# Optimization experiments

Hardware: AMD Instinct MI355X
Metric: run time of the kernel (lower is better)

## Reference

```python
import jax, jax.numpy as jnp
import numpy as np

NUM_HEADS = 16
B, S, H = 2, 8192, 1024


def setup_inputs() -> dict:
    key = jax.random.key(0)
    ks = jax.random.split(key, 6)
    scale = 1.0 / np.sqrt(H)
    return {
        "hidden_states": jax.random.normal(ks[0], (B, S, H), dtype=jnp.float32),
        "Wq": jax.random.normal(ks[1], (H, H), dtype=jnp.float32) * scale,
        "Wk": jax.random.normal(ks[2], (H, H), dtype=jnp.float32) * scale,
        "Wv": jax.random.normal(ks[3], (H, H), dtype=jnp.float32) * scale,
        "Wg": jax.random.normal(ks[4], (H, H), dtype=jnp.float32) * scale,
        "Wo": jax.random.normal(ks[5], (H, H), dtype=jnp.float32) * scale,
        "gamma": jnp.ones((H,), dtype=jnp.float32),
        "beta": jnp.zeros((H,), dtype=jnp.float32),
    }


def reference(hidden_states, Wq, Wk, Wv, Wg, Wo, gamma, beta):
    b, s, h = hidden_states.shape
    nh = NUM_HEADS
    dk = h // nh
    dv = h // nh
    # projections (bias-free linears)
    q = (hidden_states @ Wq).reshape(b, s, nh, dk)
    k = (hidden_states @ Wk).reshape(b, s, nh, dk)
    v = (hidden_states @ Wv).reshape(b, s, nh, dv)
    g = hidden_states @ Wg  # [b, s, h]
    # elu+1 feature map
    q = jax.nn.elu(q) + 1.0
    k = jax.nn.elu(k) + 1.0
    # kv = k outer v per token, then contracted with q  ==> (q.k) * v (no [b,h,n,d,e] tensor)
    qk = jnp.sum(q * k, axis=-1, keepdims=True)        # [b, s, nh, 1]
    k_sum = jnp.sum(k, axis=1, keepdims=True)          # [b, 1, nh, dk] (global over seq)
    normalizer = jnp.sum(q * k_sum, axis=-1, keepdims=True)  # [b, s, nh, 1]
    z = qk * v / (normalizer + 1e-6)                   # [b, s, nh, dv]
    z = z.reshape(b, s, nh * dv)
    # LayerNorm (eps=1e-5, affine)
    mu = jnp.mean(z, axis=-1, keepdims=True)
    var = jnp.mean(jnp.square(z - mu), axis=-1, keepdims=True)
    z = (z - mu) * jax.lax.rsqrt(var + 1e-5) * gamma + beta
    # SiLU gating and output projection
    z = z * jax.nn.silu(g)
    return z @ Wo
```

## Files before the change

kernel.cpp:

```cpp
#include <hip/hip_runtime.h>


typedef unsigned short ushort_t;
typedef unsigned int uint_t;

using short8  = __attribute__((ext_vector_type(8))) short;
using floatx4 = __attribute__((ext_vector_type(4))) float;

#define HDIM  1024
#define T_TOK 16384
#define KSPLIT 3072

__device__ __forceinline__ ushort_t f2bf(float f) {
    uint_t u = __builtin_bit_cast(uint_t, f);
    u = (u + 0x7fff + ((u >> 16) & 1)) >> 16;
    return (ushort_t)u;
}
__device__ __forceinline__ float bf2f(ushort_t h) {
    uint_t u = ((uint_t)h) << 16;
    return __builtin_bit_cast(float, u);
}
__device__ __forceinline__ void split2(float f, ushort_t& hi, ushort_t& lo) {
    hi = f2bf(f);
    lo = f2bf(f - bf2f(hi));
}
__device__ __forceinline__ void gload_lds16(const ushort_t* g, ushort_t* l) {
    __builtin_amdgcn_global_load_lds(
        (const __attribute__((address_space(1))) void*)g,
        (__attribute__((address_space(3))) void*)l, 16, 0, 0);
}

__global__ void split_w(const float* __restrict__ W0, const float* __restrict__ W1,
                        const float* __restrict__ W2, const float* __restrict__ W3,
                        const float* __restrict__ W4, ushort_t* __restrict__ WT2) {
    __shared__ float tile[32][33];
    const int z = blockIdx.z;
    const float* W = (z == 0) ? W0 : (z == 1) ? W1 : (z == 2) ? W2 : (z == 3) ? W3 : W4;
    ushort_t* dst = WT2 + (size_t)z * HDIM * 2048;
    const int n0 = blockIdx.x * 32, k0 = blockIdx.y * 32;
    const int tx = threadIdx.x & 31, ty0 = threadIdx.x >> 5;
#pragma unroll
    for (int s = 0; s < 4; ++s) {
        int ty = ty0 + 8 * s;
        tile[ty][tx] = W[(size_t)(k0 + ty) * HDIM + n0 + tx];
    }
    __syncthreads();
#pragma unroll
    for (int s = 0; s < 4; ++s) {
        int ty = ty0 + 8 * s;
        float v = tile[tx][ty];
        ushort_t hi, lo;
        split2(v, hi, lo);
        dst[(size_t)(n0 + ty) * 2048 + k0 + tx] = hi;
        dst[(size_t)(n0 + ty) * 2048 + 1024 + k0 + tx] = lo;
    }
}

__global__ __launch_bounds__(256)
void split_hidden(const float* __restrict__ h, ushort_t* __restrict__ Hs) {
    const int t = blockIdx.x;
    const int c = threadIdx.x;
    const float4 x = ((const float4*)(h + (size_t)t * HDIM))[c];
    ushort_t hi[4], lo[4];
    split2(x.x, hi[0], lo[0]); split2(x.y, hi[1], lo[1]);
    split2(x.z, hi[2], lo[2]); split2(x.w, hi[3], lo[3]);
    ushort_t* row = Hs + (size_t)t * 2048;
    uint2 hp, lp;
    hp.x = (uint_t)hi[0] | ((uint_t)hi[1] << 16);
    hp.y = (uint_t)hi[2] | ((uint_t)hi[3] << 16);
    lp.x = (uint_t)lo[0] | ((uint_t)lo[1] << 16);
    lp.y = (uint_t)lo[2] | ((uint_t)lo[3] << 16);
    *(uint2*)(row + c * 4) = hp;
    *(uint2*)(row + 1024 + c * 4) = lp;
}


#define FENCE() asm volatile("" ::: "memory")
#define VMW4()  asm volatile("s_waitcnt vmcnt(4)" ::: "memory")

#define STG_A(t, h, bsel) do { \
    const int ka_ = ((t) * 64 >= 2048) ? ((t) * 64 - 2048) : ((t) * 64); \
    gload_lds16(Ag + (size_t)((h) * 128) * 2048 + ka_, \
                &As[(bsel) * 16384 + ((h) * 128 + w * 16) * 64]); \
    gload_lds16(Ag + (size_t)((h) * 128 + 8) * 2048 + ka_, \
                &As[(bsel) * 16384 + ((h) * 128 + w * 16 + 8) * 64]); \
  } while (0)

#define STG_B(t, h, bsel) do { \
    const int kb_ = ((t) * 64 >= 1024) ? ((t) * 64 - 1024) : ((t) * 64); \
    gload_lds16(Bg + (size_t)((h) * 128) * 2048 + kb_, \
                &Bs[(bsel) * 16384 + ((h) * 128 + w * 16) * 64]); \
    gload_lds16(Bg + (size_t)((h) * 128 + 8) * 2048 + kb_, \
                &Bs[(bsel) * 16384 + ((h) * 128 + w * 16 + 8) * 64]); \
  } while (0)

#define RD_A(dst, bsel, mb, kc) do { \
    const ushort_t* _pa = ((kc) ? Ar1 : Ar0) + (bsel) * 16384; \
    _Pragma("unroll") \
    for (int _i = 0; _i < 4; ++_i) \
        dst[_i] = *(const short8*)(_pa + ((mb) + _i) * 1024); \
  } while (0)

#define RD_B(dst, bsel, kc) do { \
    const ushort_t* _pb = ((kc) ? Br1 : Br0) + (bsel) * 16384; \
    _Pragma("unroll") \
    for (int _j = 0; _j < 4; ++_j) \
        dst[_j] = *(const short8*)(_pb + _j * 1024); \
  } while (0)

#define MMX(mb, a, b) do { \
    __builtin_amdgcn_s_setprio(1); \
    _Pragma("unroll") \
    for (int _i = 0; _i < 4; ++_i) \
    _Pragma("unroll") \
    for (int _j = 0; _j < 4; ++_j) \
        acc[(mb) + _i][_j] = __builtin_amdgcn_mfma_f32_16x16x32_bf16( \
            a[_i], b[_j], acc[(mb) + _i][_j], 0, 0, 0); \
    __builtin_amdgcn_s_setprio(0); \
  } while (0)

#define TILE(t, bsel) do { \
     \
    RD_A(afB, bsel, 4, 0); \
    STG_A((t) + 1, 0, (bsel) ^ 1); STG_A((t) + 1, 1, (bsel) ^ 1); \
    MMX(0, afA, bfv0); \
     \
    RD_A(afA, bsel, 0, 1); \
    RD_B(bfv1, bsel, 1); \
    MMX(4, afB, bfv0); \
     \
    RD_A(afB, bsel, 4, 1); \
    MMX(0, afA, bfv1); \
     \
    __builtin_amdgcn_sched_barrier(0); \
    asm volatile("s_waitcnt lgkmcnt(0)" ::: "memory"); \
    FENCE(); __builtin_amdgcn_s_barrier(); FENCE(); \
    STG_B((t) + 2, 0, bsel); STG_B((t) + 2, 1, bsel); \
    VMW4(); \
    FENCE(); __builtin_amdgcn_s_barrier(); FENCE(); \
    __builtin_amdgcn_sched_barrier(0); \
     \
    RD_A(afA, (bsel) ^ 1, 0, 0); \
    RD_B(bfv0, (bsel) ^ 1, 0); \
    MMX(4, afB, bfv1); \
  } while (0)

template <int EPI>
__global__ __launch_bounds__(512, 2)
void gemm256(const ushort_t* __restrict__ A, const ushort_t* __restrict__ Bw,
             float* __restrict__ D, const float* __restrict__ kf,
             const float* __restrict__ ksum, float* __restrict__ scbuf,
             ushort_t* __restrict__ zbuf, const float* __restrict__ gamma,
             const float* __restrict__ beta) {
    __shared__ ushort_t As[2 * 256 * 64];
    __shared__ ushort_t Bs[2 * 256 * 64];
    const int tid = threadIdx.x;
    const int bx = blockIdx.x, by = blockIdx.y;
    const int w = tid >> 6, lane = tid & 63;
    const int wm = w & 1, wn = w >> 1;
    const int lrow = lane & 15, lq = lane >> 4;

    const int srow = lane >> 3;
    const int scol = ((lane & 7) ^ srow) * 8;
    const ushort_t* Ag = A + (size_t)(bx * 256 + w * 16 + srow) * 2048 + scol;
    const ushort_t* Bg = Bw + (size_t)(by * 256 + w * 16 + srow) * 2048 + scol;

    const int c0 = (lq ^ (lrow & 7)) * 8;
    const int c1 = ((lq + 4) ^ (lrow & 7)) * 8;
    const ushort_t* Ar0 = As + (wm * 128 + lrow) * 64 + c0;
    const ushort_t* Ar1 = As + (wm * 128 + lrow) * 64 + c1;
    const ushort_t* Br0 = Bs + (wn * 64 + lrow) * 64 + c0;
    const ushort_t* Br1 = Bs + (wn * 64 + lrow) * 64 + c1;

    floatx4 acc[8][4] = {};
    short8 afA[4], afB[4], bfv0[4], bfv1[4];

    STG_A(0, 0, 0); STG_A(0, 1, 0);
    STG_B(0, 0, 0); STG_B(0, 1, 0);
    STG_B(1, 0, 1); STG_B(1, 1, 1);
    VMW4();
    FENCE(); __builtin_amdgcn_s_barrier(); FENCE();
    __builtin_amdgcn_sched_barrier(0);
    RD_A(afA, 0, 0, 0);
    RD_B(bfv0, 0, 0);

#pragma unroll 1
    for (int t = 0; t < 48; t += 2) {
        TILE(t, 0);
        TILE(t + 1, 1);
    }

    const int rowbase = bx * 256 + wm * 128 + lq * 4;
    const int colbase = by * 256 + wn * 64 + lrow;

    if constexpr (EPI == 0 || EPI == 2) {
#pragma unroll
        for (int i = 0; i < 8; ++i)
#pragma unroll
            for (int j = 0; j < 4; ++j) {
                const int col = colbase + j * 16;
#pragma unroll
                for (int r = 0; r < 4; ++r) {
                    const int row = rowbase + i * 16 + r;
                    float val = acc[i][j][r];
                    if (EPI == 0) val = (val > 0.0f) ? (val + 1.0f) : (expm1f(val) + 1.0f);
                    D[(size_t)row * HDIM + col] = val;
                }
            }
    } else if constexpr (EPI == 1) {
        const int b = bx >> 5;
        float ksv[4];
#pragma unroll
        for (int j = 0; j < 4; ++j) ksv[j] = ksum[b * HDIM + colbase + j * 16];
        const int h = by * 4 + wn;
#pragma unroll
        for (int i = 0; i < 8; ++i)
#pragma unroll
            for (int r = 0; r < 4; ++r) {
                const int row = rowbase + i * 16 + r;
                float qk = 0.f, nm = 0.f;
#pragma unroll
                for (int j = 0; j < 4; ++j) {
                    float qv = acc[i][j][r];
                    qv = (qv > 0.0f) ? (qv + 1.0f) : (expm1f(qv) + 1.0f);
                    const float kv = kf[(size_t)row * HDIM + colbase + j * 16];
                    qk += qv * kv;
                    nm += qv * ksv[j];
                }
#pragma unroll
                for (int off = 1; off < 16; off <<= 1) {
                    qk += __shfl_xor(qk, off, 64);
                    nm += __shfl_xor(nm, off, 64);
                }
                if (lrow == 0) scbuf[row * 16 + h] = qk / (nm + 1e-6f);
            }
    } else {
#pragma unroll
        for (int i = 0; i < 8; ++i)
#pragma unroll
            for (int j = 0; j < 4; ++j) {
                const int col = colbase + j * 16;
                const float gam = gamma[col], bet = beta[col];
#pragma unroll
                for (int r = 0; r < 4; ++r) {
                    const int row = rowbase + i * 16 + r;
                    ushort_t* zr = zbuf + (size_t)row * 2048;
                    const float zn = bf2f(zr[col]) + bf2f(zr[1024 + col]);
                    const float g = acc[i][j][r];
                    const float sg = g / (1.0f + expf(-g));
                    ushort_t hi, lo;
                    split2((zn * gam + bet) * sg, hi, lo);
                    zr[col] = hi;
                    zr[1024 + col] = lo;
                }
            }
    }
}

template <int EPI>
__global__ __launch_bounds__(256)
void gemm_swz(const ushort_t* __restrict__ A, const ushort_t* __restrict__ Bw,
              float* __restrict__ D, const float* __restrict__ kf,
              const float* __restrict__ ksum, float* __restrict__ scbuf,
              ushort_t* __restrict__ zbuf) {
    __shared__ ushort_t As[128 * 64];
    __shared__ ushort_t Bs[128 * 64];
    const int tid = threadIdx.x;
    const int bx = blockIdx.x, by = blockIdx.y;
    const int w = tid >> 6, lane = tid & 63;
    const int wm = w & 1, wn = w >> 1;
    const int lrow = lane & 15, lq = lane >> 4;

    const int srow = lane >> 3;
    const int scol = ((lane & 7) ^ srow) * 8;
    const ushort_t* Ag = A + (size_t)(bx * 128 + w * 32 + srow) * 2048 + scol;
    const ushort_t* Bg = Bw + (size_t)(by * 128 + w * 32 + srow) * 2048 + scol;

    floatx4 acc[4][4] = {};

    for (int k0 = 0; k0 < KSPLIT; k0 += 64) {
        const int ka = k0 - ((k0 >= 2048) ? 2048 : 0);
        const int kb = k0 - ((k0 >= 1024) ? 1024 : 0);
        __syncthreads();
#pragma unroll
        for (int n = 0; n < 4; ++n) {
            gload_lds16(Ag + (size_t)(n * 8) * 2048 + ka, &As[(w * 32 + n * 8) * 64]);
            gload_lds16(Bg + (size_t)(n * 8) * 2048 + kb, &Bs[(w * 32 + n * 8) * 64]);
        }
        __syncthreads();
#pragma unroll
        for (int kk = 0; kk < 64; kk += 32) {
            short8 af[4], bf[4];
#pragma unroll
            for (int i = 0; i < 4; ++i) {
                const int c = (((kk >> 3) + lq) ^ (lrow & 7)) * 8;
                af[i] = *(const short8*)&As[(wm * 64 + i * 16 + lrow) * 64 + c];
            }
#pragma unroll
            for (int j = 0; j < 4; ++j) {
                const int c = (((kk >> 3) + lq) ^ (lrow & 7)) * 8;
                bf[j] = *(const short8*)&Bs[(wn * 64 + j * 16 + lrow) * 64 + c];
            }
#pragma unroll
            for (int i = 0; i < 4; ++i)
#pragma unroll
                for (int j = 0; j < 4; ++j)
                    acc[i][j] = __builtin_amdgcn_mfma_f32_16x16x32_bf16(af[i], bf[j], acc[i][j], 0, 0, 0);
        }
    }

    const int rowbase = bx * 128 + wm * 64 + lq * 4;
    const int colbase = by * 128 + wn * 64 + lrow;
#pragma unroll
    for (int i = 0; i < 4; ++i)
#pragma unroll
        for (int j = 0; j < 4; ++j) {
            const int col = colbase + j * 16;
#pragma unroll
            for (int r = 0; r < 4; ++r) {
                const int row = rowbase + i * 16 + r;
                float val = acc[i][j][r];
                if (EPI == 0) val = (val > 0.0f) ? (val + 1.0f) : (expm1f(val) + 1.0f);
                D[(size_t)row * HDIM + col] = val;
            }
        }
}

__global__ void ksum_partial(const float* __restrict__ kf, float* __restrict__ partial) {
    const int rg = blockIdx.x;
    const int tid = threadIdx.x;
    const float4* p = (const float4*)(kf + (size_t)rg * 64 * HDIM) + tid;
    float4 s = {0.f, 0.f, 0.f, 0.f};
    for (int r = 0; r < 64; ++r) {
        float4 x = p[(size_t)r * (HDIM / 4)];
        s.x += x.x; s.y += x.y; s.z += x.z; s.w += x.w;
    }
    ((float4*)(partial + (size_t)rg * HDIM))[tid] = s;
}
__global__ void ksum_reduce(const float* __restrict__ partial, float* __restrict__ ksum) {
    const int b = blockIdx.y;
    const int c = blockIdx.x * 256 + threadIdx.x;
    float s = 0.f;
    const float* p = partial + (size_t)b * 128 * HDIM + c;
    for (int rg = 0; rg < 128; ++rg) s += p[(size_t)rg * HDIM];
    ksum[b * HDIM + c] = s;
}

__global__ __launch_bounds__(256)
void token_lite(float* vz, const float* __restrict__ scbuf) {
    const int t = blockIdx.x;
    const int tid = threadIdx.x;
    const float4 v = ((const float4*)(vz + (size_t)t * HDIM))[tid];
    const float sc = scbuf[t * 16 + (tid >> 4)];
    float z[4] = {v.x * sc, v.y * sc, v.z * sc, v.w * sc};

    __shared__ float red[8];
    const int wv = tid >> 6, lane = tid & 63;

    float s1 = z[0] + z[1] + z[2] + z[3];
#pragma unroll
    for (int off = 1; off < 64; off <<= 1) s1 += __shfl_xor(s1, off, 64);
    if (lane == 0) red[wv] = s1;
    __syncthreads();
    const float mu = (red[0] + red[1] + red[2] + red[3]) * (1.0f / 1024.0f);

    float d[4] = {z[0] - mu, z[1] - mu, z[2] - mu, z[3] - mu};
    float s2 = d[0] * d[0] + d[1] * d[1] + d[2] * d[2] + d[3] * d[3];
#pragma unroll
    for (int off = 1; off < 64; off <<= 1) s2 += __shfl_xor(s2, off, 64);
    __syncthreads();
    if (lane == 0) red[4 + wv] = s2;
    __syncthreads();
    const float var = (red[4] + red[5] + red[6] + red[7]) * (1.0f / 1024.0f);
    const float rstd = rsqrtf(var + 1e-5f);

    ushort_t* zrow = (ushort_t*)(vz + (size_t)t * HDIM);
    ushort_t hi[4], lo[4];
#pragma unroll
    for (int c = 0; c < 4; ++c) split2(d[c] * rstd, hi[c], lo[c]);
    uint2 hp, lp;
    hp.x = (uint_t)hi[0] | ((uint_t)hi[1] << 16);
    hp.y = (uint_t)hi[2] | ((uint_t)hi[3] << 16);
    lp.x = (uint_t)lo[0] | ((uint_t)lo[1] << 16);
    lp.y = (uint_t)lo[2] | ((uint_t)lo[3] << 16);
    *(uint2*)(zrow + tid * 4) = hp;
    *(uint2*)(zrow + 1024 + tid * 4) = lp;
}

template <int VAR>
__global__ __launch_bounds__(256, 2)
void gemm_split(const float* __restrict__ A,
                const ushort_t* __restrict__ B0, const ushort_t* __restrict__ B1,
                const ushort_t* __restrict__ B2,
                float* __restrict__ D0, float* __restrict__ D1, float* __restrict__ D2,
                int K) {
    __shared__ ushort_t Ah[128 * 72];
    __shared__ ushort_t Al[128 * 72];
    __shared__ ushort_t Bh[128 * 72];
    __shared__ ushort_t Bl[128 * 72];
    const int tid = threadIdx.x;
    const int bx = blockIdx.x, by = blockIdx.y;
    const ushort_t* Bt;
    float* D;
    int n0;
    bool act;
    if (VAR == 1) {
        const int wsel = by >> 3;
        Bt = (wsel == 0) ? B0 : (wsel == 1) ? B1 : B2;
        D = (wsel == 0) ? D0 : (wsel == 1) ? D1 : D2;
        n0 = (by & 7) * 128;
        act = (wsel == 0);
    } else {
        Bt = B0; D = D0; n0 = by * 128; act = true;
    }
    const int w = tid >> 6, lane = tid & 63;
    const int wm = w & 1, wn = w >> 1;
    const int lrow = lane & 15, lq = lane >> 4;
    const int srow = tid >> 1;
    const int shalf = (tid & 1) * 32;
    const float* Arow = A + (size_t)(bx * 128 + srow) * K;
    const ushort_t* Brow = Bt + (size_t)(n0 + srow) * 2048;
    floatx4 acc[4][4] = {};
    for (int k0 = 0; k0 < K; k0 += 64) {
        float4 afr[8];
        uint4 bhr[4], blr[4];
#pragma unroll
        for (int g = 0; g < 4; ++g) {
            afr[2 * g]     = *(const float4*)(Arow + k0 + shalf + g * 8);
            afr[2 * g + 1] = *(const float4*)(Arow + k0 + shalf + g * 8 + 4);
            bhr[g] = *(const uint4*)(Brow + k0 + shalf + g * 8);
            blr[g] = *(const uint4*)(Brow + 1024 + k0 + shalf + g * 8);
        }
        __syncthreads();
#pragma unroll
        for (int g = 0; g < 4; ++g) {
            ushort_t h[8], l[8];
            const float4 f0 = afr[2 * g], f1 = afr[2 * g + 1];
            split2(f0.x, h[0], l[0]); split2(f0.y, h[1], l[1]);
            split2(f0.z, h[2], l[2]); split2(f0.w, h[3], l[3]);
            split2(f1.x, h[4], l[4]); split2(f1.y, h[5], l[5]);
            split2(f1.z, h[6], l[6]); split2(f1.w, h[7], l[7]);
            uint4 hp, lp;
            hp.x = (uint_t)h[0] | ((uint_t)h[1] << 16);
            hp.y = (uint_t)h[2] | ((uint_t)h[3] << 16);
            hp.z = (uint_t)h[4] | ((uint_t)h[5] << 16);
            hp.w = (uint_t)h[6] | ((uint_t)h[7] << 16);
            lp.x = (uint_t)l[0] | ((uint_t)l[1] << 16);
            lp.y = (uint_t)l[2] | ((uint_t)l[3] << 16);
            lp.z = (uint_t)l[4] | ((uint_t)l[5] << 16);
            lp.w = (uint_t)l[6] | ((uint_t)l[7] << 16);
            *(uint4*)&Ah[srow * 72 + shalf + g * 8] = hp;
            *(uint4*)&Al[srow * 72 + shalf + g * 8] = lp;
            *(uint4*)&Bh[srow * 72 + shalf + g * 8] = bhr[g];
            *(uint4*)&Bl[srow * 72 + shalf + g * 8] = blr[g];
        }
        __syncthreads();
#pragma unroll
        for (int kk = 0; kk < 64; kk += 32) {
            short8 ah[4], bh[4], xl[4];
#pragma unroll
            for (int i = 0; i < 4; ++i)
                ah[i] = *(const short8*)&Ah[(wm * 64 + i * 16 + lrow) * 72 + kk + lq * 8];
#pragma unroll
            for (int j = 0; j < 4; ++j)
                bh[j] = *(const short8*)&Bh[(wn * 64 + j * 16 + lrow) * 72 + kk + lq * 8];
#pragma unroll
            for (int i = 0; i < 4; ++i)
#pragma unroll
                for (int j = 0; j < 4; ++j)
                    acc[i][j] = __builtin_amdgcn_mfma_f32_16x16x32_bf16(ah[i], bh[j], acc[i][j], 0, 0, 0);
#pragma unroll
            for (int i = 0; i < 4; ++i)
                xl[i] = *(const short8*)&Al[(wm * 64 + i * 16 + lrow) * 72 + kk + lq * 8];
#pragma unroll
            for (int i = 0; i < 4; ++i)
#pragma unroll
                for (int j = 0; j < 4; ++j)
                    acc[i][j] = __builtin_amdgcn_mfma_f32_16x16x32_bf16(xl[i], bh[j], acc[i][j], 0, 0, 0);
#pragma unroll
            for (int j = 0; j < 4; ++j)
                xl[j] = *(const short8*)&Bl[(wn * 64 + j * 16 + lrow) * 72 + kk + lq * 8];
#pragma unroll
            for (int i = 0; i < 4; ++i)
#pragma unroll
                for (int j = 0; j < 4; ++j)
                    acc[i][j] = __builtin_amdgcn_mfma_f32_16x16x32_bf16(ah[i], xl[j], acc[i][j], 0, 0, 0);
        }
    }
    const int rowbase = bx * 128 + wm * 64 + lq * 4;
    const int colbase = n0 + wn * 64 + lrow;
#pragma unroll
    for (int i = 0; i < 4; ++i)
#pragma unroll
        for (int j = 0; j < 4; ++j) {
            const int col = colbase + j * 16;
#pragma unroll
            for (int r = 0; r < 4; ++r) {
                const int row = rowbase + i * 16 + r;
                float val = acc[i][j][r];
                if (act) val = (val > 0.0f) ? (val + 1.0f) : (expm1f(val) + 1.0f);
                D[(size_t)row * HDIM + col] = val;
            }
        }
}

__global__ __launch_bounds__(256)
void token_f32(const float* __restrict__ qd, const float* __restrict__ vd,
               const float* __restrict__ gd, float* kz,
               const float* __restrict__ ksum,
               const float* __restrict__ gamma, const float* __restrict__ beta,
               int chunk_base) {
    const int tl = blockIdx.x;
    const int t = chunk_base + tl;
    const int b = t >> 13;
    const int tid = threadIdx.x;
    const float4 q = ((const float4*)(qd + (size_t)tl * HDIM))[tid];
    const float4 k = ((const float4*)(kz + (size_t)t * HDIM))[tid];
    const float4 v = ((const float4*)(vd + (size_t)tl * HDIM))[tid];
    const float4 ks = ((const float4*)(ksum + (size_t)b * HDIM))[tid];
    float qk = q.x * k.x + q.y * k.y + q.z * k.z + q.w * k.w;
    float nm = q.x * ks.x + q.y * ks.y + q.z * ks.z + q.w * ks.w;
#pragma unroll
    for (int off = 1; off < 16; off <<= 1) {
        qk += __shfl_xor(qk, off, 64);
        nm += __shfl_xor(nm, off, 64);
    }
    const float sc = qk / (nm + 1e-6f);
    float z[4] = {v.x * sc, v.y * sc, v.z * sc, v.w * sc};
    __shared__ float red[8];
    const int wv = tid >> 6, lane = tid & 63;
    float s1 = z[0] + z[1] + z[2] + z[3];
#pragma unroll
    for (int off = 1; off < 64; off <<= 1) s1 += __shfl_xor(s1, off, 64);
    if (lane == 0) red[wv] = s1;
    __syncthreads();
    const float mu = (red[0] + red[1] + red[2] + red[3]) * (1.0f / 1024.0f);
    float d[4] = {z[0] - mu, z[1] - mu, z[2] - mu, z[3] - mu};
    float s2 = d[0] * d[0] + d[1] * d[1] + d[2] * d[2] + d[3] * d[3];
#pragma unroll
    for (int off = 1; off < 64; off <<= 1) s2 += __shfl_xor(s2, off, 64);
    __syncthreads();
    if (lane == 0) red[4 + wv] = s2;
    __syncthreads();
    const float var = (red[4] + red[5] + red[6] + red[7]) * (1.0f / 1024.0f);
    const float rstd = rsqrtf(var + 1e-5f);
    const float4 gm = ((const float4*)gamma)[tid];
    const float4 bt = ((const float4*)beta)[tid];
    const float4 g = ((const float4*)(gd + (size_t)tl * HDIM))[tid];
    const float gv[4] = {g.x, g.y, g.z, g.w};
    const float gmv[4] = {gm.x, gm.y, gm.z, gm.w};
    const float btv[4] = {bt.x, bt.y, bt.z, bt.w};
    ushort_t hi[4], lo[4];
#pragma unroll
    for (int c = 0; c < 4; ++c) {
        const float zn = d[c] * rstd * gmv[c] + btv[c];
        const float sg = gv[c] / (1.0f + expf(-gv[c]));
        split2(zn * sg, hi[c], lo[c]);
    }
    ushort_t* zrow = (ushort_t*)(kz + (size_t)t * HDIM);
    uint2 hp, lp;
    hp.x = (uint_t)hi[0] | ((uint_t)hi[1] << 16);
    hp.y = (uint_t)hi[2] | ((uint_t)hi[3] << 16);
    lp.x = (uint_t)lo[0] | ((uint_t)lo[1] << 16);
    lp.y = (uint_t)lo[2] | ((uint_t)lo[3] << 16);
    *(uint2*)(zrow + tid * 4) = hp;
    *(uint2*)(zrow + 1024 + tid * 4) = lp;
}

extern "C" void kernel_launch(void* const* d_in, const int* in_sizes, int n_in,
                              void* d_out, int out_size, void* d_ws, size_t ws_size,
                              hipStream_t stream) {
    const float* hidden = (const float*)d_in[0];
    const float* Wq = (const float*)d_in[1];
    const float* Wk = (const float*)d_in[2];
    const float* Wv = (const float*)d_in[3];
    const float* Wg = (const float*)d_in[4];
    const float* Wo = (const float*)d_in[5];
    const float* gamma = (const float*)d_in[6];
    const float* beta = (const float*)d_in[7];

    char* w = (char*)d_ws;
    float* kb = (float*)w;            w += (size_t)67108864;
    ushort_t* WT2 = (ushort_t*)w;     w += (size_t)20971520;
    float* partial = (float*)w;       w += (size_t)1048576;
    float* ksum = (float*)w;          w += (size_t)8192;
    float* scbuf = (float*)w;         w += (size_t)1048576;
    const size_t base = (size_t)(w - (char*)d_ws);

    ushort_t* Wk2 = WT2;
    ushort_t* Wq2 = WT2 + (size_t)1 * HDIM * 2048;
    ushort_t* Wv2 = WT2 + (size_t)2 * HDIM * 2048;
    ushort_t* Wg2 = WT2 + (size_t)3 * HDIM * 2048;
    ushort_t* Wo2 = WT2 + (size_t)4 * HDIM * 2048;

    split_w<<<dim3(32, 32, 5), 256, 0, stream>>>(Wk, Wq, Wv, Wg, Wo, WT2);

    if (ws_size >= base + 67108864ull) {
        ushort_t* Hs = (ushort_t*)w;
        split_hidden<<<dim3(T_TOK), 256, 0, stream>>>(hidden, Hs);
        gemm256<0><<<dim3(64, 4), 512, 0, stream>>>(Hs, Wk2, kb, nullptr, nullptr,
                                                    nullptr, nullptr, nullptr, nullptr);
        ksum_partial<<<dim3(256), 256, 0, stream>>>(kb, partial);
        ksum_reduce<<<dim3(4, 2), 256, 0, stream>>>(partial, ksum);
        gemm256<1><<<dim3(64, 4), 512, 0, stream>>>(Hs, Wq2, nullptr, kb, ksum,
                                                    scbuf, nullptr, nullptr, nullptr);
        gemm256<2><<<dim3(64, 4), 512, 0, stream>>>(Hs, Wv2, kb, nullptr, nullptr,
                                                    nullptr, nullptr, nullptr, nullptr);
        token_lite<<<dim3(T_TOK), 256, 0, stream>>>(kb, scbuf);
        gemm256<3><<<dim3(64, 4), 512, 0, stream>>>(Hs, Wg2, nullptr, nullptr, nullptr,
                                                    nullptr, (ushort_t*)kb, gamma, beta);
        gemm256<2><<<dim3(64, 4), 512, 0, stream>>>((const ushort_t*)kb, Wo2,
                                                    (float*)d_out, nullptr, nullptr,
                                                    nullptr, nullptr, nullptr, nullptr);
    } else {
        const int C = 2048;
        float* qc = (float*)w;
        float* vc = qc + (size_t)C * HDIM;
        float* gc = vc + (size_t)C * HDIM;
        gemm_split<0><<<dim3(128, 8), 256, 0, stream>>>(hidden, Wk2, nullptr, nullptr,
                                                        kb, nullptr, nullptr, HDIM);
        ksum_partial<<<dim3(256), 256, 0, stream>>>(kb, partial);
        ksum_reduce<<<dim3(4, 2), 256, 0, stream>>>(partial, ksum);
        for (int c = 0; c < 8; ++c) {
            const float* Ac = hidden + (size_t)c * C * HDIM;
            gemm_split<1><<<dim3(C / 128, 24), 256, 0, stream>>>(Ac, Wq2, Wv2, Wg2,
                                                                 qc, vc, gc, HDIM);
            token_f32<<<dim3(C), 256, 0, stream>>>(qc, vc, gc, kb, ksum,
                                                   gamma, beta, c * C);
        }
        gemm_swz<2><<<dim3(128, 8), 256, 0, stream>>>((const ushort_t*)kb, Wo2,
                                                      (float*)d_out, nullptr, nullptr,
                                                      nullptr, nullptr);
    }
}
```

Baseline: 693.9 us.

## Load B operand fragments directly from global into registers, dropping B LDS staging

The GEMM main loop stops staging the B tile through shared memory and instead has each wave load its B MFMA fragments straight from global memory into registers, double-buffered across k-halves. This removes the B LDS buffer, its barrier and lgkm wait, and halves LDS usage, which could allow higher occupancy and less LDS traffic. In exchange, B data is no longer shared between the two M-waves through LDS, so global and L2 traffic rises. Register loads that are not fully coalesced can also expose more global latency in the loop.

```diff
diff --git a/kernel.cpp b/kernel.cpp
--- a/kernel.cpp
+++ b/kernel.cpp
@@ -77,6 +77,7 @@
 
 #define FENCE() asm volatile("" ::: "memory")
 #define VMW4()  asm volatile("s_waitcnt vmcnt(4)" ::: "memory")
+#define SB()    __builtin_amdgcn_sched_barrier(0)
 
 #define STG_A(t, h, bsel) do { \
     const int ka_ = ((t) * 64 >= 2048) ? ((t) * 64 - 2048) : ((t) * 64); \
@@ -86,12 +87,11 @@
                 &As[(bsel) * 16384 + ((h) * 128 + w * 16 + 8) * 64]); \
   } while (0)
 
-#define STG_B(t, h, bsel) do { \
+#define GL_B(dst, t, kc) do { \
     const int kb_ = ((t) * 64 >= 1024) ? ((t) * 64 - 1024) : ((t) * 64); \
-    gload_lds16(Bg + (size_t)((h) * 128) * 2048 + kb_, \
-                &Bs[(bsel) * 16384 + ((h) * 128 + w * 16) * 64]); \
-    gload_lds16(Bg + (size_t)((h) * 128 + 8) * 2048 + kb_, \
-                &Bs[(bsel) * 16384 + ((h) * 128 + w * 16 + 8) * 64]); \
+    _Pragma("unroll") \
+    for (int _j = 0; _j < 4; ++_j) \
+        dst[_j] = *(const short8*)(Bgr + (size_t)(_j * 16) * 2048 + kb_ + (kc) * 32); \
   } while (0)
 
 #define RD_A(dst, bsel, mb, kc) do { \
@@ -99,13 +99,6 @@
     _Pragma("unroll") \
     for (int _i = 0; _i < 4; ++_i) \
         dst[_i] = *(const short8*)(_pa + ((mb) + _i) * 1024); \
-  } while (0)
-
-#define RD_B(dst, bsel, kc) do { \
-    const ushort_t* _pb = ((kc) ? Br1 : Br0) + (bsel) * 16384; \
-    _Pragma("unroll") \
-    for (int _j = 0; _j < 4; ++_j) \
-        dst[_j] = *(const short8*)(_pb + _j * 1024); \
   } while (0)
 
 #define MMX(mb, a, b) do { \
@@ -121,28 +114,24 @@
 
 #define TILE(t, bsel) do { \
      \
+    GL_B(bf1, (t), 1); \
     RD_A(afB, bsel, 4, 0); \
-    STG_A((t) + 1, 0, (bsel) ^ 1); STG_A((t) + 1, 1, (bsel) ^ 1); \
-    MMX(0, afA, bfv0); \
+    STG_A((t) + 1, 0, (bsel) ^ 1); \
+    MMX(0, afA, bf0); \
+    RD_A(afA, bsel, 0, 1); \
+    STG_A((t) + 1, 1, (bsel) ^ 1); \
+    MMX(4, afB, bf0); \
      \
-    RD_A(afA, bsel, 0, 1); \
-    RD_B(bfv1, bsel, 1); \
-    MMX(4, afB, bfv0); \
+    SB(); \
      \
+    GL_B(bf0, (t) + 1, 0); \
     RD_A(afB, bsel, 4, 1); \
-    MMX(0, afA, bfv1); \
-     \
-    __builtin_amdgcn_sched_barrier(0); \
-    asm volatile("s_waitcnt lgkmcnt(0)" ::: "memory"); \
-    FENCE(); __builtin_amdgcn_s_barrier(); FENCE(); \
-    STG_B((t) + 2, 0, bsel); STG_B((t) + 2, 1, bsel); \
+    MMX(0, afA, bf1); \
+    MMX(4, afB, bf1); \
     VMW4(); \
     FENCE(); __builtin_amdgcn_s_barrier(); FENCE(); \
-    __builtin_amdgcn_sched_barrier(0); \
-     \
+    SB(); \
     RD_A(afA, (bsel) ^ 1, 0, 0); \
-    RD_B(bfv0, (bsel) ^ 1, 0); \
-    MMX(4, afB, bfv1); \
   } while (0)
 
 template <int EPI>
@@ -153,7 +142,6 @@
              ushort_t* __restrict__ zbuf, const float* __restrict__ gamma,
              const float* __restrict__ beta) {
     __shared__ ushort_t As[2 * 256 * 64];
-    __shared__ ushort_t Bs[2 * 256 * 64];
     const int tid = threadIdx.x;
     const int bx = blockIdx.x, by = blockIdx.y;
     const int w = tid >> 6, lane = tid & 63;
@@ -163,26 +151,24 @@
     const int srow = lane >> 3;
     const int scol = ((lane & 7) ^ srow) * 8;
     const ushort_t* Ag = A + (size_t)(bx * 256 + w * 16 + srow) * 2048 + scol;
-    const ushort_t* Bg = Bw + (size_t)(by * 256 + w * 16 + srow) * 2048 + scol;
+    const ushort_t* Bgr = Bw + (size_t)(by * 256 + wn * 64 + lrow) * 2048 + lq * 8;
 
     const int c0 = (lq ^ (lrow & 7)) * 8;
     const int c1 = ((lq + 4) ^ (lrow & 7)) * 8;
     const ushort_t* Ar0 = As + (wm * 128 + lrow) * 64 + c0;
     const ushort_t* Ar1 = As + (wm * 128 + lrow) * 64 + c1;
-    const ushort_t* Br0 = Bs + (wn * 64 + lrow) * 64 + c0;
-    const ushort_t* Br1 = Bs + (wn * 64 + lrow) * 64 + c1;
 
     floatx4 acc[8][4] = {};
-    short8 afA[4], afB[4], bfv0[4], bfv1[4];
+    short8 afA[4], afB[4], bf0[4], bf1[4];
 
     STG_A(0, 0, 0); STG_A(0, 1, 0);
-    STG_B(0, 0, 0); STG_B(0, 1, 0);
-    STG_B(1, 0, 1); STG_B(1, 1, 1);
+    SB();
+    GL_B(bf0, 0, 0);
+    SB();
     VMW4();
     FENCE(); __builtin_amdgcn_s_barrier(); FENCE();
-    __builtin_amdgcn_sched_barrier(0);
+    SB();
     RD_A(afA, 0, 0, 0);
-    RD_B(bfv0, 0, 0);
 
 #pragma unroll 1
     for (int t = 0; t < 48; t += 2) {
```

After: 774.3 us. 1.12x slower.
